# Kernel tuning notes

Hardware: AMD Instinct MI355X
Metric: run time of the kernel (lower is better)

## Reference

```python
import jax, jax.numpy as jnp
import numpy as np

N_NODES = 100000
BASE_DIM = 128
E1 = 500000
E2 = 250000
N_TYPES = 4


def setup_inputs() -> dict:
    key = jax.random.key(0)
    ks = jax.random.split(key, 9)
    x = jax.random.normal(ks[0], (N_NODES, BASE_DIM), dtype=jnp.float32)
    # per-edge-type dense transforms (shape-1: d->d, shape-2: 2d->d)
    W1 = jax.random.normal(ks[1], (N_TYPES, BASE_DIM, BASE_DIM), dtype=jnp.float32) * 0.05
    W2 = jax.random.normal(ks[2], (N_TYPES, 2 * BASE_DIM, BASE_DIM), dtype=jnp.float32) * 0.05
    src1 = jax.random.randint(ks[3], (E1,), 0, N_NODES, dtype=jnp.int32)
    tgt1 = jax.random.randint(ks[4], (E1,), 0, N_NODES, dtype=jnp.int32)
    type1 = jax.random.randint(ks[5], (E1,), 0, N_TYPES, dtype=jnp.int32)
    src2 = jax.random.randint(ks[6], (2 * E2,), 0, N_NODES, dtype=jnp.int32)
    tgt2 = jax.random.randint(ks[7], (E2,), 0, N_NODES, dtype=jnp.int32)
    type2 = jax.random.randint(ks[8], (E2,), 0, N_TYPES, dtype=jnp.int32)
    return {"x": x, "W1": W1, "W2": W2, "src1": src1, "tgt1": tgt1,
            "type1": type1, "src2": src2, "tgt2": tgt2, "type2": type2}


def _gather_transform_scatter(x, W, src, tgt, etype, arity, n_nodes):
    # gather `arity` source nodes per hyperedge and concat features: (E, arity*d)
    d = x.shape[1]
    concat = x[src].reshape(-1, arity * d)
    # per-edge-type dense transform; small loop over fixed #types, masked accumulate
    acc = jnp.zeros((concat.shape[0], d), dtype=x.dtype)
    for t in range(W.shape[0]):
        acc = acc + jnp.where((etype == t)[:, None], concat @ W[t], 0.0)
    # scatter-add messages to target nodes
    return jax.ops.segment_sum(acc, tgt, num_segments=n_nodes)


def reference(x, W1, W2, src1, tgt1, type1, src2, tgt2, type2):
    n = x.shape[0]
    out = x
    out = out + _gather_transform_scatter(x, W1, src1, tgt1, type1, 1, n)
    out = out + _gather_transform_scatter(x, W2, src2, tgt2, type2, 2, n)
    return out
```

## Files before the change

kernel.cpp:

```cpp
#include <hip/hip_runtime.h>
#include <hip/hip_bf16.h>

#define D 128
#define EPB 32
#define NB 256

typedef __attribute__((ext_vector_type(8))) short bf16x8;
typedef __attribute__((ext_vector_type(4))) float f32x4;

__device__ inline unsigned short f2bf(float f) {
    union { float f; unsigned int u; } v;
    v.f = f;
    unsigned int u = v.u;
    unsigned int r = u + 0x7fffu + ((u >> 16) & 1u);
    return (unsigned short)(r >> 16);
}
__device__ inline float bf2f(unsigned short b) {
    union { unsigned int u; float f; } v;
    v.u = ((unsigned int)b) << 16;
    return v.f;
}

__global__ __launch_bounds__(256) void copy_kernel(float* __restrict__ out,
                                                   const float* __restrict__ x,
                                                   int n_elems) {
    int n4 = n_elems >> 2;
    const float4* src = (const float4*)x;
    float4* dst = (float4*)out;
    for (int i = blockIdx.x * blockDim.x + threadIdx.x; i < n4;
         i += gridDim.x * blockDim.x)
        dst[i] = src[i];
}

__global__ __launch_bounds__(256) void conv_w(const float* __restrict__ W,
                                              unsigned short* __restrict__ Wt,
                                              int K) {
    __shared__ float tile[32][33];
    int k0 = blockIdx.x * 32, c0 = blockIdx.y * 32, t = blockIdx.z;
    int tr = threadIdx.x >> 5, tc = threadIdx.x & 31;
#pragma unroll
    for (int m = 0; m < 4; m++)
        tile[m * 8 + tr][tc] = W[((size_t)t * K + k0 + m * 8 + tr) * D + c0 + tc];
    __syncthreads();
#pragma unroll
    for (int m = 0; m < 4; m++)
        Wt[((size_t)t * D + c0 + m * 8 + tr) * K + k0 + tc] = f2bf(tile[tc][m * 8 + tr]);
}

__global__ __launch_bounds__(256) void hist_types(const int* __restrict__ type,
                                                  int n, int* __restrict__ hist) {
    __shared__ int h[4];
    if (threadIdx.x < 4) h[threadIdx.x] = 0;
    __syncthreads();
    for (int i = blockIdx.x * 256 + threadIdx.x; i < n; i += NB * 256)
        atomicAdd(&h[type[i]], 1);
    __syncthreads();
    if (threadIdx.x < 4) hist[blockIdx.x * 4 + threadIdx.x] = h[threadIdx.x];
}

__global__ void scan_offsets(int* __restrict__ meta,
                             const int* __restrict__ hist1, int* __restrict__ off1,
                             const int* __restrict__ hist2, int* __restrict__ off2) {
    int t = threadIdx.x;
    if (t < 4) {
        int s = 0;
        for (int b = 0; b < NB; b++) s += hist1[b * 4 + t];
        meta[t] = s;
    } else if (t < 8) {
        int tt = t - 4, s = 0;
        for (int b = 0; b < NB; b++) s += hist2[b * 4 + tt];
        meta[4 + tt] = s;
    }
    __syncthreads();
    if (t == 0) {
        int p = 0;
        for (int k = 0; k < 4; k++) {
            meta[8 + k] = p;
            p += ((meta[k] + EPB - 1) / EPB) * EPB;
        }
        meta[12] = p;
        p = 0;
        for (int k = 0; k < 4; k++) {
            meta[13 + k] = p;
            p += ((meta[4 + k] + EPB - 1) / EPB) * EPB;
        }
        meta[17] = p;
    }
    __syncthreads();
    if (t < 4) {
        int p = meta[8 + t];
        for (int b = 0; b < NB; b++) { off1[b * 4 + t] = p; p += hist1[b * 4 + t]; }
    } else if (t < 8) {
        int tt = t - 4;
        int p = meta[13 + tt];
        for (int b = 0; b < NB; b++) { off2[b * 4 + tt] = p; p += hist2[b * 4 + tt]; }
    }
}

__global__ __launch_bounds__(256) void write_sorted(const int* __restrict__ type,
                                                    int n,
                                                    const int* __restrict__ off,
                                                    int* __restrict__ sorted) {
    __shared__ int loff[4];
    if (threadIdx.x < 4) loff[threadIdx.x] = off[blockIdx.x * 4 + threadIdx.x];
    __syncthreads();
    for (int i = blockIdx.x * 256 + threadIdx.x; i < n; i += NB * 256) {
        int t = type[i];
        int pos = atomicAdd(&loff[t], 1);
        sorted[pos] = i;
    }
}

__global__ __launch_bounds__(256) void assign_rel(const int* __restrict__ tgt, int n,
                                                  int* __restrict__ cnt,
                                                  int* __restrict__ pos) {
    for (int i = blockIdx.x * blockDim.x + threadIdx.x; i < n;
         i += gridDim.x * blockDim.x)
        pos[i] = atomicAdd(&cnt[tgt[i]], 1);
}

__global__ __launch_bounds__(256) void scan_pass1(const int* __restrict__ cnt, int n,
                                                  int* __restrict__ base,
                                                  int* __restrict__ bsum) {
    __shared__ int s[256];
    int b = blockIdx.x, t = threadIdx.x;
    int i0 = b * 512 + 2 * t;
    int v0 = (i0 < n) ? cnt[i0] : 0;
    int v1 = (i0 + 1 < n) ? cnt[i0 + 1] : 0;
    s[t] = v0 + v1;
    __syncthreads();
    for (int off = 1; off < 256; off <<= 1) {
        int v = s[t];
        int u = (t >= off) ? s[t - off] : 0;
        __syncthreads();
        s[t] = v + u;
        __syncthreads();
    }
    int excl = (t > 0) ? s[t - 1] : 0;
    if (i0 < n) base[i0] = excl;
    if (i0 + 1 < n) base[i0 + 1] = excl + v0;
    if (t == 255) bsum[b] = s[255];
}

__global__ __launch_bounds__(256) void scan_pass2(int* __restrict__ bsum, int nb) {
    __shared__ int s[256];
    int t = threadIdx.x;
    int run = 0;
    for (int b0 = 0; b0 < nb; b0 += 256) {
        int v = (b0 + t < nb) ? bsum[b0 + t] : 0;
        s[t] = v;
        __syncthreads();
        for (int off = 1; off < 256; off <<= 1) {
            int a = s[t];
            int u = (t >= off) ? s[t - off] : 0;
            __syncthreads();
            s[t] = a + u;
            __syncthreads();
        }
        if (b0 + t < nb) bsum[b0 + t] = run + ((t > 0) ? s[t - 1] : 0);
        int tot = s[255];
        __syncthreads();
        run += tot;
    }
    if (t == 0) bsum[nb] = run;
}

__global__ __launch_bounds__(256) void scan_pass3(int* __restrict__ base,
                                                  const int* __restrict__ bsum, int n) {
    int i = blockIdx.x * 256 + threadIdx.x;
    if (i < n) base[i] += bsum[i >> 9];
    else if (i == n) base[n] = bsum[(n + 511) >> 9];
}

__global__ __launch_bounds__(256) void edge1_msg(
    const float* __restrict__ x, const unsigned short* __restrict__ Wt1,
    const int* __restrict__ src, const int* __restrict__ tgt,
    const int* __restrict__ sorted, const int* __restrict__ meta,
    const int* __restrict__ basep, const int* __restrict__ pos,
    unsigned short* __restrict__ msg) {
    __shared__ uint4 As4[512];
    __shared__ int s_mrow[EPB];
    __shared__ int s_src[EPB];
    char* As = (char*)As4;

    int tid = threadIdx.x;
    int g0 = blockIdx.x * EPB;
    const int* pb = meta + 8;
    int t = 0;
#pragma unroll
    for (int k = 1; k < 4; k++)
        if (g0 >= pb[k]) t = k;
    const unsigned short* __restrict__ W = Wt1 + (size_t)t * D * D;

    if (tid < EPB) {
        int eid = sorted[g0 + tid];
        int sv = -1, mr = -1;
        if (eid >= 0) { sv = src[eid]; mr = basep[tgt[eid]] + pos[eid]; }
        s_src[tid] = sv;
        s_mrow[tid] = mr;
    }
    __syncthreads();

    {
        int r = tid >> 3, u0 = tid & 7;
        int sv = s_src[r];
        const float4* srow = (const float4*)(x + (size_t)sv * D);
#pragma unroll
        for (int q = 0; q < 4; q++) {
            int u = u0 + 8 * q;
            float4 v = make_float4(0.f, 0.f, 0.f, 0.f);
            if (sv >= 0) v = srow[u];
            uint2 p;
            p.x = (unsigned)f2bf(v.x) | ((unsigned)f2bf(v.y) << 16);
            p.y = (unsigned)f2bf(v.z) | ((unsigned)f2bf(v.w) << 16);
            int byte = ((((u >> 1) * 16) ^ ((r & 7) << 4)) + (u & 1) * 8);
            *(uint2*)(As + r * 256 + byte) = p;
        }
    }
    __syncthreads();

    int wave = tid >> 6, lane = tid & 63;
    int c0 = wave * 32;
    int lrow = lane & 15, lgrp = lane >> 4;

    bf16x8 b[2][4];
#pragma unroll
    for (int fc = 0; fc < 2; fc++)
#pragma unroll
        for (int kk = 0; kk < 4; kk++)
            b[fc][kk] = *(const bf16x8*)(W + (size_t)(c0 + fc * 16 + lrow) * D +
                                         kk * 32 + lgrp * 8);

    f32x4 acc[2][2];
#pragma unroll
    for (int i = 0; i < 2; i++)
#pragma unroll
        for (int j = 0; j < 2; j++) acc[i][j] = (f32x4){0.f, 0.f, 0.f, 0.f};

#pragma unroll
    for (int kk = 0; kk < 4; kk++) {
        bf16x8 a0, a1;
        {
            int r = lrow;
            a0 = *(const bf16x8*)(As + r * 256 +
                                  ((kk * 64 + lgrp * 16) ^ ((r & 7) << 4)));
        }
        {
            int r = 16 + lrow;
            a1 = *(const bf16x8*)(As + r * 256 +
                                  ((kk * 64 + lgrp * 16) ^ ((r & 7) << 4)));
        }
        acc[0][0] = __builtin_amdgcn_mfma_f32_16x16x32_bf16(a0, b[0][kk], acc[0][0], 0, 0, 0);
        acc[1][0] = __builtin_amdgcn_mfma_f32_16x16x32_bf16(a1, b[0][kk], acc[1][0], 0, 0, 0);
        acc[0][1] = __builtin_amdgcn_mfma_f32_16x16x32_bf16(a0, b[1][kk], acc[0][1], 0, 0, 0);
        acc[1][1] = __builtin_amdgcn_mfma_f32_16x16x32_bf16(a1, b[1][kk], acc[1][1], 0, 0, 0);
    }

#pragma unroll
    for (int fr = 0; fr < 2; fr++)
#pragma unroll
        for (int reg = 0; reg < 4; reg++) {
            int erow = fr * 16 + lgrp * 4 + reg;
            int mr = s_mrow[erow];
            if (mr >= 0) {
#pragma unroll
                for (int fc = 0; fc < 2; fc++)
                    msg[(size_t)mr * D + c0 + fc * 16 + lrow] =
                        f2bf(acc[fr][fc][reg]);
            }
        }
}

__global__ __launch_bounds__(256) void edge2_msg(
    const float* __restrict__ x, const unsigned short* __restrict__ Wt2,
    const int* __restrict__ src2, const int* __restrict__ tgt,
    const int* __restrict__ sorted, const int* __restrict__ meta,
    const int* __restrict__ basep, const int* __restrict__ pos,
    unsigned short* __restrict__ msg) {
    __shared__ uint4 As4[1024];
    __shared__ int s_mrow[EPB];
    __shared__ int s_srcA[EPB];
    __shared__ int s_srcB[EPB];
    char* As = (char*)As4;

    int tid = threadIdx.x;
    int g0 = blockIdx.x * EPB;
    const int* pb = meta + 13;
    int t = 0;
#pragma unroll
    for (int k = 1; k < 4; k++)
        if (g0 >= pb[k]) t = k;
    const unsigned short* __restrict__ W = Wt2 + (size_t)t * D * 2 * D;

    if (tid < EPB) {
        int eid = sorted[g0 + tid];
        int sa = -1, sb = -1, mr = -1;
        if (eid >= 0) {
            sa = src2[2 * eid];
            sb = src2[2 * eid + 1];
            mr = basep[tgt[eid]] + pos[eid];
        }
        s_srcA[tid] = sa;
        s_srcB[tid] = sb;
        s_mrow[tid] = mr;
    }
    __syncthreads();

    {
        int r = tid >> 3, u0 = tid & 7;
        int sa = s_srcA[r], sb = s_srcB[r];
        const float4* rowA = (const float4*)(x + (size_t)sa * D);
        const float4* rowB = (const float4*)(x + (size_t)sb * D);
#pragma unroll
        for (int q = 0; q < 8; q++) {
            int u = u0 + 8 * q;
            float4 v = make_float4(0.f, 0.f, 0.f, 0.f);
            if (sa >= 0) v = (u < 32) ? rowA[u] : rowB[u - 32];
            uint2 p;
            p.x = (unsigned)f2bf(v.x) | ((unsigned)f2bf(v.y) << 16);
            p.y = (unsigned)f2bf(v.z) | ((unsigned)f2bf(v.w) << 16);
            int byte = ((((u >> 1) * 16) ^ ((r & 7) << 4)) + (u & 1) * 8);
            *(uint2*)(As + r * 512 + byte) = p;
        }
    }
    __syncthreads();

    int wave = tid >> 6, lane = tid & 63;
    int c0 = wave * 32;
    int lrow = lane & 15, lgrp = lane >> 4;

    f32x4 acc[2][2];
#pragma unroll
    for (int i = 0; i < 2; i++)
#pragma unroll
        for (int j = 0; j < 2; j++) acc[i][j] = (f32x4){0.f, 0.f, 0.f, 0.f};

#pragma unroll
    for (int kk = 0; kk < 8; kk++) {
        bf16x8 b0 = *(const bf16x8*)(W + (size_t)(c0 + lrow) * 2 * D + kk * 32 + lgrp * 8);
        bf16x8 b1 = *(const bf16x8*)(W + (size_t)(c0 + 16 + lrow) * 2 * D + kk * 32 + lgrp * 8);
        bf16x8 a0, a1;
        {
            int r = lrow;
            a0 = *(const bf16x8*)(As + r * 512 +
                                  ((kk * 64 + lgrp * 16) ^ ((r & 7) << 4)));
        }
        {
            int r = 16 + lrow;
            a1 = *(const bf16x8*)(As + r * 512 +
                                  ((kk * 64 + lgrp * 16) ^ ((r & 7) << 4)));
        }
        acc[0][0] = __builtin_amdgcn_mfma_f32_16x16x32_bf16(a0, b0, acc[0][0], 0, 0, 0);
        acc[1][0] = __builtin_amdgcn_mfma_f32_16x16x32_bf16(a1, b0, acc[1][0], 0, 0, 0);
        acc[0][1] = __builtin_amdgcn_mfma_f32_16x16x32_bf16(a0, b1, acc[0][1], 0, 0, 0);
        acc[1][1] = __builtin_amdgcn_mfma_f32_16x16x32_bf16(a1, b1, acc[1][1], 0, 0, 0);
    }

#pragma unroll
    for (int fr = 0; fr < 2; fr++)
#pragma unroll
        for (int reg = 0; reg < 4; reg++) {
            int erow = fr * 16 + lgrp * 4 + reg;
            int mr = s_mrow[erow];
            if (mr >= 0) {
#pragma unroll
                for (int fc = 0; fc < 2; fc++)
                    msg[(size_t)mr * D + c0 + fc * 16 + lrow] =
                        f2bf(acc[fr][fc][reg]);
            }
        }
}

__global__ __launch_bounds__(256) void finalize(
    const float* __restrict__ x, const unsigned short* __restrict__ msg,
    const int* __restrict__ basep, float* __restrict__ out, int nn) {
    int wib = threadIdx.x >> 6, lane = threadIdx.x & 63;
    for (int v = blockIdx.x * 4 + wib; v < nn; v += gridDim.x * 4) {
        int b0 = basep[v], b1 = basep[v + 1];
        float2 xv = *(const float2*)(x + (size_t)v * D + lane * 2);
        float a0 = xv.x, a1 = xv.y;
        for (int i = b0; i < b1; i++) {
            unsigned u = *(const unsigned*)(msg + (size_t)i * D + lane * 2);
            a0 += bf2f((unsigned short)(u & 0xffff));
            a1 += bf2f((unsigned short)(u >> 16));
        }
        *(float2*)(out + (size_t)v * D + lane * 2) = make_float2(a0, a1);
    }
}

__global__ __launch_bounds__(256) void edge1_mfma(
    const float* __restrict__ x, const unsigned short* __restrict__ Wt1,
    const int* __restrict__ src, const int* __restrict__ tgt,
    const int* __restrict__ sorted, const int* __restrict__ meta,
    float* __restrict__ out) {
    __shared__ uint4 As4[512];
    __shared__ int s_tgt[EPB];
    __shared__ int s_src[EPB];
    char* As = (char*)As4;

    int tid = threadIdx.x;
    int g0 = blockIdx.x * EPB;
    const int* pb = meta + 8;
    int t = 0;
#pragma unroll
    for (int k = 1; k < 4; k++)
        if (g0 >= pb[k]) t = k;
    const unsigned short* __restrict__ W = Wt1 + (size_t)t * D * D;

    if (tid < EPB) {
        int eid = sorted[g0 + tid];
        int sv = -1, tv = -1;
        if (eid >= 0) { sv = src[eid]; tv = tgt[eid]; }
        s_src[tid] = sv;
        s_tgt[tid] = tv;
    }
    __syncthreads();
    {
        int r = tid >> 3, u0 = tid & 7;
        int sv = s_src[r];
        const float4* srow = (const float4*)(x + (size_t)sv * D);
#pragma unroll
        for (int q = 0; q < 4; q++) {
            int u = u0 + 8 * q;
            float4 v = make_float4(0.f, 0.f, 0.f, 0.f);
            if (sv >= 0) v = srow[u];
            uint2 p;
            p.x = (unsigned)f2bf(v.x) | ((unsigned)f2bf(v.y) << 16);
            p.y = (unsigned)f2bf(v.z) | ((unsigned)f2bf(v.w) << 16);
            int byte = ((((u >> 1) * 16) ^ ((r & 7) << 4)) + (u & 1) * 8);
            *(uint2*)(As + r * 256 + byte) = p;
        }
    }
    __syncthreads();

    int wave = tid >> 6, lane = tid & 63;
    int c0 = wave * 32;
    int lrow = lane & 15, lgrp = lane >> 4;

    bf16x8 b[2][4];
#pragma unroll
    for (int fc = 0; fc < 2; fc++)
#pragma unroll
        for (int kk = 0; kk < 4; kk++)
            b[fc][kk] = *(const bf16x8*)(W + (size_t)(c0 + fc * 16 + lrow) * D +
                                         kk * 32 + lgrp * 8);

    f32x4 acc[2][2];
#pragma unroll
    for (int i = 0; i < 2; i++)
#pragma unroll
        for (int j = 0; j < 2; j++) acc[i][j] = (f32x4){0.f, 0.f, 0.f, 0.f};

#pragma unroll
    for (int kk = 0; kk < 4; kk++) {
        bf16x8 a0, a1;
        {
            int r = lrow;
            a0 = *(const bf16x8*)(As + r * 256 + ((kk * 64 + lgrp * 16) ^ ((r & 7) << 4)));
        }
        {
            int r = 16 + lrow;
            a1 = *(const bf16x8*)(As + r * 256 + ((kk * 64 + lgrp * 16) ^ ((r & 7) << 4)));
        }
        acc[0][0] = __builtin_amdgcn_mfma_f32_16x16x32_bf16(a0, b[0][kk], acc[0][0], 0, 0, 0);
        acc[1][0] = __builtin_amdgcn_mfma_f32_16x16x32_bf16(a1, b[0][kk], acc[1][0], 0, 0, 0);
        acc[0][1] = __builtin_amdgcn_mfma_f32_16x16x32_bf16(a0, b[1][kk], acc[0][1], 0, 0, 0);
        acc[1][1] = __builtin_amdgcn_mfma_f32_16x16x32_bf16(a1, b[1][kk], acc[1][1], 0, 0, 0);
    }

#pragma unroll
    for (int fr = 0; fr < 2; fr++)
#pragma unroll
        for (int reg = 0; reg < 4; reg++) {
            int erow = fr * 16 + lgrp * 4 + reg;
            int tv = s_tgt[erow];
            if (tv >= 0) {
#pragma unroll
                for (int fc = 0; fc < 2; fc++)
                    atomicAdd(&out[(size_t)tv * D + c0 + fc * 16 + lrow],
                              acc[fr][fc][reg]);
            }
        }
}

__global__ __launch_bounds__(256) void edge2_mfma(
    const float* __restrict__ x, const unsigned short* __restrict__ Wt2,
    const int* __restrict__ src2, const int* __restrict__ tgt,
    const int* __restrict__ sorted, const int* __restrict__ meta,
    float* __restrict__ out) {
    __shared__ uint4 As4[1024];
    __shared__ int s_tgt[EPB];
    __shared__ int s_srcA[EPB];
    __shared__ int s_srcB[EPB];
    char* As = (char*)As4;

    int tid = threadIdx.x;
    int g0 = blockIdx.x * EPB;
    const int* pb = meta + 13;
    int t = 0;
#pragma unroll
    for (int k = 1; k < 4; k++)
        if (g0 >= pb[k]) t = k;
    const unsigned short* __restrict__ W = Wt2 + (size_t)t * D * 2 * D;

    if (tid < EPB) {
        int eid = sorted[g0 + tid];
        int sa = -1, sb = -1, tv = -1;
        if (eid >= 0) { sa = src2[2 * eid]; sb = src2[2 * eid + 1]; tv = tgt[eid]; }
        s_srcA[tid] = sa;
        s_srcB[tid] = sb;
        s_tgt[tid] = tv;
    }
    __syncthreads();
    {
        int r = tid >> 3, u0 = tid & 7;
        int sa = s_srcA[r], sb = s_srcB[r];
        const float4* rowA = (const float4*)(x + (size_t)sa * D);
        const float4* rowB = (const float4*)(x + (size_t)sb * D);
#pragma unroll
        for (int q = 0; q < 8; q++) {
            int u = u0 + 8 * q;
            float4 v = make_float4(0.f, 0.f, 0.f, 0.f);
            if (sa >= 0) v = (u < 32) ? rowA[u] : rowB[u - 32];
            uint2 p;
            p.x = (unsigned)f2bf(v.x) | ((unsigned)f2bf(v.y) << 16);
            p.y = (unsigned)f2bf(v.z) | ((unsigned)f2bf(v.w) << 16);
            int byte = ((((u >> 1) * 16) ^ ((r & 7) << 4)) + (u & 1) * 8);
            *(uint2*)(As + r * 512 + byte) = p;
        }
    }
    __syncthreads();

    int wave = tid >> 6, lane = tid & 63;
    int c0 = wave * 32;
    int lrow = lane & 15, lgrp = lane >> 4;

    f32x4 acc[2][2];
#pragma unroll
    for (int i = 0; i < 2; i++)
#pragma unroll
        for (int j = 0; j < 2; j++) acc[i][j] = (f32x4){0.f, 0.f, 0.f, 0.f};

#pragma unroll
    for (int kk = 0; kk < 8; kk++) {
        bf16x8 b0 = *(const bf16x8*)(W + (size_t)(c0 + lrow) * 2 * D + kk * 32 + lgrp * 8);
        bf16x8 b1 = *(const bf16x8*)(W + (size_t)(c0 + 16 + lrow) * 2 * D + kk * 32 + lgrp * 8);
        bf16x8 a0, a1;
        {
            int r = lrow;
            a0 = *(const bf16x8*)(As + r * 512 + ((kk * 64 + lgrp * 16) ^ ((r & 7) << 4)));
        }
        {
            int r = 16 + lrow;
            a1 = *(const bf16x8*)(As + r * 512 + ((kk * 64 + lgrp * 16) ^ ((r & 7) << 4)));
        }
        acc[0][0] = __builtin_amdgcn_mfma_f32_16x16x32_bf16(a0, b0, acc[0][0], 0, 0, 0);
        acc[1][0] = __builtin_amdgcn_mfma_f32_16x16x32_bf16(a1, b0, acc[1][0], 0, 0, 0);
        acc[0][1] = __builtin_amdgcn_mfma_f32_16x16x32_bf16(a0, b1, acc[0][1], 0, 0, 0);
        acc[1][1] = __builtin_amdgcn_mfma_f32_16x16x32_bf16(a1, b1, acc[1][1], 0, 0, 0);
    }

#pragma unroll
    for (int fr = 0; fr < 2; fr++)
#pragma unroll
        for (int reg = 0; reg < 4; reg++) {
            int erow = fr * 16 + lgrp * 4 + reg;
            int tv = s_tgt[erow];
            if (tv >= 0) {
#pragma unroll
                for (int fc = 0; fc < 2; fc++)
                    atomicAdd(&out[(size_t)tv * D + c0 + fc * 16 + lrow],
                              acc[fr][fc][reg]);
            }
        }
}

__global__ __launch_bounds__(256) void e1_simple(
    const float* __restrict__ x, const float* __restrict__ W1,
    const int* __restrict__ src, const int* __restrict__ tgt,
    const int* __restrict__ type, float* __restrict__ out, int n) {
    int lane = threadIdx.x & 63;
    int wid = (blockIdx.x * blockDim.x + threadIdx.x) >> 6;
    int nw = (gridDim.x * blockDim.x) >> 6;
    for (int e = wid; e < n; e += nw) {
        const float* W = W1 + (size_t)type[e] * D * D;
        const float* xr = x + (size_t)src[e] * D;
        float a0 = 0.f, a1 = 0.f;
        for (int i = 0; i < D; i++) {
            float xv = xr[i];
            a0 = fmaf(xv, W[i * D + lane], a0);
            a1 = fmaf(xv, W[i * D + 64 + lane], a1);
        }
        atomicAdd(&out[(size_t)tgt[e] * D + lane], a0);
        atomicAdd(&out[(size_t)tgt[e] * D + 64 + lane], a1);
    }
}

__global__ __launch_bounds__(256) void e2_simple(
    const float* __restrict__ x, const float* __restrict__ W2,
    const int* __restrict__ src2, const int* __restrict__ tgt,
    const int* __restrict__ type, float* __restrict__ out, int n) {
    int lane = threadIdx.x & 63;
    int wid = (blockIdx.x * blockDim.x + threadIdx.x) >> 6;
    int nw = (gridDim.x * blockDim.x) >> 6;
    for (int e = wid; e < n; e += nw) {
        const float* W = W2 + (size_t)type[e] * 2 * D * D;
        const float* xrA = x + (size_t)src2[2 * e] * D;
        const float* xrB = x + (size_t)src2[2 * e + 1] * D;
        float a0 = 0.f, a1 = 0.f;
        for (int i = 0; i < 2 * D; i++) {
            float xv = (i < D) ? xrA[i] : xrB[i - D];
            a0 = fmaf(xv, W[i * D + lane], a0);
            a1 = fmaf(xv, W[i * D + 64 + lane], a1);
        }
        atomicAdd(&out[(size_t)tgt[e] * D + lane], a0);
        atomicAdd(&out[(size_t)tgt[e] * D + 64 + lane], a1);
    }
}

extern "C" void kernel_launch(void* const* d_in, const int* in_sizes, int n_in,
                              void* d_out, int out_size, void* d_ws, size_t ws_size,
                              hipStream_t stream) {
    const float* x = (const float*)d_in[0];
    const float* W1 = (const float*)d_in[1];
    const float* W2 = (const float*)d_in[2];
    const int* src1 = (const int*)d_in[3];
    const int* tgt1 = (const int*)d_in[4];
    const int* type1 = (const int*)d_in[5];
    const int* src2 = (const int*)d_in[6];
    const int* tgt2 = (const int*)d_in[7];
    const int* type2 = (const int*)d_in[8];
    float* out = (float*)d_out;

    int nn = in_sizes[0] / D;
    int E1c = in_sizes[3];
    int E2c = in_sizes[7];

    int grid1 = (E1c + 4 * (EPB - 1) + EPB - 1) / EPB;
    int grid2 = (E2c + 4 * (EPB - 1) + EPB - 1) / EPB;
    int cap1 = grid1 * EPB;
    int cap2 = grid2 * EPB;
    int nb_scan = (nn + 511) / 512;

    size_t o_meta = 0;
    size_t o_hist1 = o_meta + 32;
    size_t o_off1 = o_hist1 + (size_t)NB * 4;
    size_t o_hist2 = o_off1 + (size_t)NB * 4;
    size_t o_off2 = o_hist2 + (size_t)NB * 4;
    size_t o_sorted1 = o_off2 + (size_t)NB * 4;
    size_t o_sorted2 = o_sorted1 + cap1;
    size_t o_pos1 = o_sorted2 + cap2;
    size_t o_pos2 = o_pos1 + E1c;
    size_t o_cnt = o_pos2 + E2c;
    size_t o_base = o_cnt + nn;
    size_t o_bsum = o_base + nn + 1;
    size_t ints_full = o_bsum + nb_scan + 1;
    size_t ints_r3 = o_pos1;

    size_t w1_elems = (size_t)4 * D * D;
    size_t w2_elems = (size_t)4 * D * 2 * D;

    size_t wb_full = (ints_full * 4 + 255) & ~(size_t)255;
    size_t wb_r3 = (ints_r3 * 4 + 255) & ~(size_t)255;
    size_t wt_bytes = (w1_elems + w2_elems) * 2;

    size_t msg_off = (wb_full + wt_bytes + 255) & ~(size_t)255;
    size_t msg_bytes = (size_t)(E1c + E2c) * D * 2;
    size_t need_full = msg_off + msg_bytes;
    size_t need_r3 = wb_r3 + wt_bytes;

    if (ws_size >= need_full) {
        int* wsI = (int*)d_ws;
        int* meta = wsI + o_meta;
        int* hist1 = wsI + o_hist1;
        int* off1 = wsI + o_off1;
        int* hist2 = wsI + o_hist2;
        int* off2 = wsI + o_off2;
        int* sorted1 = wsI + o_sorted1;
        int* sorted2 = wsI + o_sorted2;
        int* pos1 = wsI + o_pos1;
        int* pos2 = wsI + o_pos2;
        int* cnt = wsI + o_cnt;
        int* basep = wsI + o_base;
        int* bsum = wsI + o_bsum;
        unsigned short* wt1 = (unsigned short*)((char*)d_ws + wb_full);
        unsigned short* wt2 = wt1 + w1_elems;
        unsigned short* msg = (unsigned short*)((char*)d_ws + msg_off);

        hipMemsetAsync(sorted1, 0xFF, (size_t)4 * (cap1 + cap2), stream);
        hipMemsetAsync(cnt, 0, (size_t)4 * nn, stream);

        conv_w<<<dim3(4, 4, 4), 256, 0, stream>>>(W1, wt1, D);
        conv_w<<<dim3(8, 4, 4), 256, 0, stream>>>(W2, wt2, 2 * D);

        hist_types<<<NB, 256, 0, stream>>>(type1, E1c, hist1);
        hist_types<<<NB, 256, 0, stream>>>(type2, E2c, hist2);
        scan_offsets<<<1, 64, 0, stream>>>(meta, hist1, off1, hist2, off2);
        write_sorted<<<NB, 256, 0, stream>>>(type1, E1c, off1, sorted1);
        write_sorted<<<NB, 256, 0, stream>>>(type2, E2c, off2, sorted2);

        assign_rel<<<2048, 256, 0, stream>>>(tgt1, E1c, cnt, pos1);
        assign_rel<<<2048, 256, 0, stream>>>(tgt2, E2c, cnt, pos2);
        scan_pass1<<<nb_scan, 256, 0, stream>>>(cnt, nn, basep, bsum);
        scan_pass2<<<1, 256, 0, stream>>>(bsum, nb_scan);
        scan_pass3<<<(nn + 1 + 255) / 256, 256, 0, stream>>>(basep, bsum, nn);

        edge1_msg<<<grid1, 256, 0, stream>>>(x, wt1, src1, tgt1, sorted1, meta,
                                             basep, pos1, msg);
        edge2_msg<<<grid2, 256, 0, stream>>>(x, wt2, src2, tgt2, sorted2, meta,
                                             basep, pos2, msg);

        finalize<<<(nn + 3) / 4, 256, 0, stream>>>(x, msg, basep, out, nn);
    } else if (ws_size >= need_r3) {
        int* wsI = (int*)d_ws;
        int* meta = wsI + o_meta;
        int* hist1 = wsI + o_hist1;
        int* off1 = wsI + o_off1;
        int* hist2 = wsI + o_hist2;
        int* off2 = wsI + o_off2;
        int* sorted1 = wsI + o_sorted1;
        int* sorted2 = wsI + o_sorted2;
        unsigned short* wt1 = (unsigned short*)((char*)d_ws + wb_r3);
        unsigned short* wt2 = wt1 + w1_elems;

        copy_kernel<<<2048, 256, 0, stream>>>(out, x, nn * D);
        hipMemsetAsync(sorted1, 0xFF, (size_t)4 * (cap1 + cap2), stream);

        conv_w<<<dim3(4, 4, 4), 256, 0, stream>>>(W1, wt1, D);
        conv_w<<<dim3(8, 4, 4), 256, 0, stream>>>(W2, wt2, 2 * D);

        hist_types<<<NB, 256, 0, stream>>>(type1, E1c, hist1);
        hist_types<<<NB, 256, 0, stream>>>(type2, E2c, hist2);
        scan_offsets<<<1, 64, 0, stream>>>(meta, hist1, off1, hist2, off2);
        write_sorted<<<NB, 256, 0, stream>>>(type1, E1c, off1, sorted1);
        write_sorted<<<NB, 256, 0, stream>>>(type2, E2c, off2, sorted2);

        edge1_mfma<<<grid1, 256, 0, stream>>>(x, wt1, src1, tgt1, sorted1, meta, out);
        edge2_mfma<<<grid2, 256, 0, stream>>>(x, wt2, src2, tgt2, sorted2, meta, out);
    } else {
        copy_kernel<<<2048, 256, 0, stream>>>(out, x, nn * D);
        e1_simple<<<2048, 256, 0, stream>>>(x, W1, src1, tgt1, type1, out, E1c);
        e2_simple<<<2048, 256, 0, stream>>>(x, W2, src2, tgt2, type2, out, E2c);
    }
}
```

Measured before the change: 344.0 us.

## Precompute per-node transformed tables for all types, then gather per target

Result: no change. 345.2 us (+0.3%).

```diff
diff --git a/kernel.cpp b/kernel.cpp
--- a/kernel.cpp
+++ b/kernel.cpp
@@ -20,6 +20,8 @@
     v.u = ((unsigned int)b) << 16;
     return v.f;
 }
+__device__ inline float bflo(unsigned u) { return bf2f((unsigned short)(u & 0xffff)); }
+__device__ inline float bfhi(unsigned u) { return bf2f((unsigned short)(u >> 16)); }
 
 __global__ __launch_bounds__(256) void copy_kernel(float* __restrict__ out,
                                                    const float* __restrict__ x,
@@ -172,6 +174,164 @@
     else if (i == n) base[n] = bsum[(n + 511) >> 9];
 }
 
+#define RMASK ((1 << 27) - 1)
+__global__ __launch_bounds__(256) void write_rec1(
+    const int* __restrict__ src, const int* __restrict__ tgt,
+    const int* __restrict__ type, int n, const int* __restrict__ base,
+    const int* __restrict__ pos, int* __restrict__ rec) {
+    for (int i = blockIdx.x * blockDim.x + threadIdx.x; i < n;
+         i += gridDim.x * blockDim.x)
+        rec[base[tgt[i]] + pos[i]] = src[i] | (type[i] << 27);
+}
+
+__global__ __launch_bounds__(256) void write_rec2(
+    const int* __restrict__ src2, const int* __restrict__ tgt,
+    const int* __restrict__ type, int n, const int* __restrict__ base,
+    const int* __restrict__ pos, int* __restrict__ reca, int* __restrict__ recb) {
+    for (int i = blockIdx.x * blockDim.x + threadIdx.x; i < n;
+         i += gridDim.x * blockDim.x) {
+        int s = base[tgt[i]] + pos[i];
+        reca[s] = src2[2 * i] | (type[i] << 27);
+        recb[s] = src2[2 * i + 1];
+    }
+}
+
+__global__ __launch_bounds__(256) void dense12(
+    const float* __restrict__ x, const unsigned short* __restrict__ wt1,
+    const unsigned short* __restrict__ wt2, unsigned short* __restrict__ tabs,
+    int nn) {
+    __shared__ uint4 As4[2048];
+    char* As = (char*)As4;
+    int tid = threadIdx.x;
+    int m0 = blockIdx.x * 128;
+
+    {
+        int r = tid >> 1;
+        int u0 = tid & 1;
+        int node = m0 + r;
+        bool ok = node < nn;
+        const float4* srow = (const float4*)(x + (size_t)node * D);
+#pragma unroll
+        for (int q = 0; q < 16; q++) {
+            int u = u0 + 2 * q;
+            float4 v = make_float4(0.f, 0.f, 0.f, 0.f);
+            if (ok) v = srow[u];
+            uint2 p;
+            p.x = (unsigned)f2bf(v.x) | ((unsigned)f2bf(v.y) << 16);
+            p.y = (unsigned)f2bf(v.z) | ((unsigned)f2bf(v.w) << 16);
+            int byte = ((((u >> 1) * 16) ^ ((r & 7) << 4)) + (u & 1) * 8);
+            *(uint2*)(As + r * 256 + byte) = p;
+        }
+    }
+    __syncthreads();
+
+    int wave = tid >> 6, lane = tid & 63;
+    int lrow = lane & 15, lgrp = lane >> 4;
+    int r0 = wave * 32;
+
+    bf16x8 a[2][4];
+#pragma unroll
+    for (int fr = 0; fr < 2; fr++)
+#pragma unroll
+        for (int kk = 0; kk < 4; kk++) {
+            int rr = r0 + fr * 16 + lrow;
+            a[fr][kk] = *(const bf16x8*)(As + rr * 256 +
+                                         ((kk * 64 + lgrp * 16) ^ ((rr & 7) << 4)));
+        }
+
+    for (int g = 0; g < 12; g++) {
+        int t = g & 3;
+        const unsigned short* W;
+        int K, koff;
+        if (g < 4) { W = wt1 + (size_t)t * D * D; K = D; koff = 0; }
+        else if (g < 8) { W = wt2 + (size_t)t * D * 2 * D; K = 2 * D; koff = 0; }
+        else { W = wt2 + (size_t)t * D * 2 * D; K = 2 * D; koff = D; }
+        unsigned short* tab = tabs + (size_t)g * nn * D;
+
+        for (int cf = 0; cf < 4; cf++) {
+            int c0 = cf * 32;
+            bf16x8 b[2][4];
+#pragma unroll
+            for (int fc = 0; fc < 2; fc++)
+#pragma unroll
+                for (int kk = 0; kk < 4; kk++)
+                    b[fc][kk] = *(const bf16x8*)(W + (size_t)(c0 + fc * 16 + lrow) * K +
+                                                 koff + kk * 32 + lgrp * 8);
+            f32x4 acc[2][2];
+#pragma unroll
+            for (int i = 0; i < 2; i++)
+#pragma unroll
+                for (int j = 0; j < 2; j++) acc[i][j] = (f32x4){0.f, 0.f, 0.f, 0.f};
+#pragma unroll
+            for (int kk = 0; kk < 4; kk++) {
+                acc[0][0] = __builtin_amdgcn_mfma_f32_16x16x32_bf16(a[0][kk], b[0][kk], acc[0][0], 0, 0, 0);
+                acc[1][0] = __builtin_amdgcn_mfma_f32_16x16x32_bf16(a[1][kk], b[0][kk], acc[1][0], 0, 0, 0);
+                acc[0][1] = __builtin_amdgcn_mfma_f32_16x16x32_bf16(a[0][kk], b[1][kk], acc[0][1], 0, 0, 0);
+                acc[1][1] = __builtin_amdgcn_mfma_f32_16x16x32_bf16(a[1][kk], b[1][kk], acc[1][1], 0, 0, 0);
+            }
+#pragma unroll
+            for (int fr = 0; fr < 2; fr++)
+#pragma unroll
+                for (int reg = 0; reg < 4; reg++) {
+                    int node = m0 + r0 + fr * 16 + lgrp * 4 + reg;
+                    if (node < nn) {
+#pragma unroll
+                        for (int fc = 0; fc < 2; fc++)
+                            tab[(size_t)node * D + c0 + fc * 16 + lrow] =
+                                f2bf(acc[fr][fc][reg]);
+                    }
+                }
+        }
+    }
+}
+
+__global__ __launch_bounds__(256) void gather_fin(
+    const float* __restrict__ x, const unsigned short* __restrict__ tabs,
+    const int* __restrict__ base1, const int* __restrict__ rec1,
+    const int* __restrict__ base2, const int* __restrict__ rec2a,
+    const int* __restrict__ rec2b, float* __restrict__ out, int nn) {
+    int wib = threadIdx.x >> 6, lane = threadIdx.x & 63;
+    for (int v = blockIdx.x * 4 + wib; v < nn; v += gridDim.x * 4) {
+        float2 xv = *(const float2*)(x + (size_t)v * D + lane * 2);
+        float a0 = xv.x, a1 = xv.y;
+
+        int b0 = base1[v], b1 = base1[v + 1];
+        int i = b0;
+        for (; i + 1 < b1; i += 2) {
+            int r0 = rec1[i], r1 = rec1[i + 1];
+            const unsigned short* p0 =
+                tabs + ((size_t)(unsigned)(r0 >> 27) * nn + (r0 & RMASK)) * D;
+            const unsigned short* p1 =
+                tabs + ((size_t)(unsigned)(r1 >> 27) * nn + (r1 & RMASK)) * D;
+            unsigned u0 = *(const unsigned*)(p0 + lane * 2);
+            unsigned u1 = *(const unsigned*)(p1 + lane * 2);
+            a0 += bflo(u0) + bflo(u1);
+            a1 += bfhi(u0) + bfhi(u1);
+        }
+        if (i < b1) {
+            int r0 = rec1[i];
+            const unsigned short* p0 =
+                tabs + ((size_t)(unsigned)(r0 >> 27) * nn + (r0 & RMASK)) * D;
+            unsigned u0 = *(const unsigned*)(p0 + lane * 2);
+            a0 += bflo(u0);
+            a1 += bfhi(u0);
+        }
+
+        int c0 = base2[v], c1 = base2[v + 1];
+        for (int j = c0; j < c1; j++) {
+            int ra = rec2a[j], sb = rec2b[j];
+            int t = (int)((unsigned)ra >> 27), sa = ra & RMASK;
+            const unsigned short* pu = tabs + ((size_t)(4 + t) * nn + sa) * D;
+            const unsigned short* pl = tabs + ((size_t)(8 + t) * nn + sb) * D;
+            unsigned uu = *(const unsigned*)(pu + lane * 2);
+            unsigned ul = *(const unsigned*)(pl + lane * 2);
+            a0 += bflo(uu) + bflo(ul);
+            a1 += bfhi(uu) + bfhi(ul);
+        }
+        *(float2*)(out + (size_t)v * D + lane * 2) = make_float2(a0, a1);
+    }
+}
+
 __global__ __launch_bounds__(256) void edge1_msg(
     const float* __restrict__ x, const unsigned short* __restrict__ Wt1,
     const int* __restrict__ src, const int* __restrict__ tgt,
@@ -200,7 +360,6 @@
         s_mrow[tid] = mr;
     }
     __syncthreads();
-
     {
         int r = tid >> 3, u0 = tid & 7;
         int sv = s_src[r];
@@ -242,13 +401,11 @@
         bf16x8 a0, a1;
         {
             int r = lrow;
-            a0 = *(const bf16x8*)(As + r * 256 +
-                                  ((kk * 64 + lgrp * 16) ^ ((r & 7) << 4)));
+            a0 = *(const bf16x8*)(As + r * 256 + ((kk * 64 + lgrp * 16) ^ ((r & 7) << 4)));
         }
         {
             int r = 16 + lrow;
-            a1 = *(const bf16x8*)(As + r * 256 +
-                                  ((kk * 64 + lgrp * 16) ^ ((r & 7) << 4)));
+            a1 = *(const bf16x8*)(As + r * 256 + ((kk * 64 + lgrp * 16) ^ ((r & 7) << 4)));
         }
         acc[0][0] = __builtin_amdgcn_mfma_f32_16x16x32_bf16(a0, b[0][kk], acc[0][0], 0, 0, 0);
         acc[1][0] = __builtin_amdgcn_mfma_f32_16x16x32_bf16(a1, b[0][kk], acc[1][0], 0, 0, 0);
@@ -265,8 +422,7 @@
             if (mr >= 0) {
 #pragma unroll
                 for (int fc = 0; fc < 2; fc++)
-                    msg[(size_t)mr * D + c0 + fc * 16 + lrow] =
-                        f2bf(acc[fr][fc][reg]);
+                    msg[(size_t)mr * D + c0 + fc * 16 + lrow] = f2bf(acc[fr][fc][reg]);
             }
         }
 }
@@ -305,7 +461,6 @@
         s_mrow[tid] = mr;
     }
     __syncthreads();
-
     {
         int r = tid >> 3, u0 = tid & 7;
         int sa = s_srcA[r], sb = s_srcB[r];
@@ -342,13 +497,11 @@
         bf16x8 a0, a1;
         {
             int r = lrow;
-            a0 = *(const bf16x8*)(As + r * 512 +
-                                  ((kk * 64 + lgrp * 16) ^ ((r & 7) << 4)));
+            a0 = *(const bf16x8*)(As + r * 512 + ((kk * 64 + lgrp * 16) ^ ((r & 7) << 4)));
         }
         {
             int r = 16 + lrow;
-            a1 = *(const bf16x8*)(As + r * 512 +
-                                  ((kk * 64 + lgrp * 16) ^ ((r & 7) << 4)));
+            a1 = *(const bf16x8*)(As + r * 512 + ((kk * 64 + lgrp * 16) ^ ((r & 7) << 4)));
         }
         acc[0][0] = __builtin_amdgcn_mfma_f32_16x16x32_bf16(a0, b0, acc[0][0], 0, 0, 0);
         acc[1][0] = __builtin_amdgcn_mfma_f32_16x16x32_bf16(a1, b0, acc[1][0], 0, 0, 0);
@@ -365,8 +518,7 @@
             if (mr >= 0) {
 #pragma unroll
                 for (int fc = 0; fc < 2; fc++)
-                    msg[(size_t)mr * D + c0 + fc * 16 + lrow] =
-                        f2bf(acc[fr][fc][reg]);
+                    msg[(size_t)mr * D + c0 + fc * 16 + lrow] = f2bf(acc[fr][fc][reg]);
             }
         }
 }
@@ -381,198 +533,11 @@
         float a0 = xv.x, a1 = xv.y;
         for (int i = b0; i < b1; i++) {
             unsigned u = *(const unsigned*)(msg + (size_t)i * D + lane * 2);
-            a0 += bf2f((unsigned short)(u & 0xffff));
-            a1 += bf2f((unsigned short)(u >> 16));
+            a0 += bflo(u);
+            a1 += bfhi(u);
         }
         *(float2*)(out + (size_t)v * D + lane * 2) = make_float2(a0, a1);
     }
-}
-
-__global__ __launch_bounds__(256) void edge1_mfma(
-    const float* __restrict__ x, const unsigned short* __restrict__ Wt1,
-    const int* __restrict__ src, const int* __restrict__ tgt,
-    const int* __restrict__ sorted, const int* __restrict__ meta,
-    float* __restrict__ out) {
-    __shared__ uint4 As4[512];
-    __shared__ int s_tgt[EPB];
-    __shared__ int s_src[EPB];
-    char* As = (char*)As4;
-
-    int tid = threadIdx.x;
-    int g0 = blockIdx.x * EPB;
-    const int* pb = meta + 8;
-    int t = 0;
-#pragma unroll
-    for (int k = 1; k < 4; k++)
-        if (g0 >= pb[k]) t = k;
-    const unsigned short* __restrict__ W = Wt1 + (size_t)t * D * D;
-
-    if (tid < EPB) {
-        int eid = sorted[g0 + tid];
-        int sv = -1, tv = -1;
-        if (eid >= 0) { sv = src[eid]; tv = tgt[eid]; }
-        s_src[tid] = sv;
-        s_tgt[tid] = tv;
-    }
-    __syncthreads();
-    {
-        int r = tid >> 3, u0 = tid & 7;
-        int sv = s_src[r];
-        const float4* srow = (const float4*)(x + (size_t)sv * D);
-#pragma unroll
-        for (int q = 0; q < 4; q++) {
-            int u = u0 + 8 * q;
-            float4 v = make_float4(0.f, 0.f, 0.f, 0.f);
-            if (sv >= 0) v = srow[u];
-            uint2 p;
-            p.x = (unsigned)f2bf(v.x) | ((unsigned)f2bf(v.y) << 16);
-            p.y = (unsigned)f2bf(v.z) | ((unsigned)f2bf(v.w) << 16);
-            int byte = ((((u >> 1) * 16) ^ ((r & 7) << 4)) + (u & 1) * 8);
-            *(uint2*)(As + r * 256 + byte) = p;
-        }
-    }
-    __syncthreads();
-
-    int wave = tid >> 6, lane = tid & 63;
-    int c0 = wave * 32;
-    int lrow = lane & 15, lgrp = lane >> 4;
-
-    bf16x8 b[2][4];
-#pragma unroll
-    for (int fc = 0; fc < 2; fc++)
-#pragma unroll
-        for (int kk = 0; kk < 4; kk++)
-            b[fc][kk] = *(const bf16x8*)(W + (size_t)(c0 + fc * 16 + lrow) * D +
-                                         kk * 32 + lgrp * 8);
-
-    f32x4 acc[2][2];
-#pragma unroll
-    for (int i = 0; i < 2; i++)
-#pragma unroll
-        for (int j = 0; j < 2; j++) acc[i][j] = (f32x4){0.f, 0.f, 0.f, 0.f};
-
-#pragma unroll
-    for (int kk = 0; kk < 4; kk++) {
-        bf16x8 a0, a1;
-        {
-            int r = lrow;
-            a0 = *(const bf16x8*)(As + r * 256 + ((kk * 64 + lgrp * 16) ^ ((r & 7) << 4)));
-        }
-        {
-            int r = 16 + lrow;
-            a1 = *(const bf16x8*)(As + r * 256 + ((kk * 64 + lgrp * 16) ^ ((r & 7) << 4)));
-        }
-        acc[0][0] = __builtin_amdgcn_mfma_f32_16x16x32_bf16(a0, b[0][kk], acc[0][0], 0, 0, 0);
-        acc[1][0] = __builtin_amdgcn_mfma_f32_16x16x32_bf16(a1, b[0][kk], acc[1][0], 0, 0, 0);
-        acc[0][1] = __builtin_amdgcn_mfma_f32_16x16x32_bf16(a0, b[1][kk], acc[0][1], 0, 0, 0);
-        acc[1][1] = __builtin_amdgcn_mfma_f32_16x16x32_bf16(a1, b[1][kk], acc[1][1], 0, 0, 0);
-    }
-
-#pragma unroll
-    for (int fr = 0; fr < 2; fr++)
-#pragma unroll
-        for (int reg = 0; reg < 4; reg++) {
-            int erow = fr * 16 + lgrp * 4 + reg;
-            int tv = s_tgt[erow];
-            if (tv >= 0) {
-#pragma unroll
-                for (int fc = 0; fc < 2; fc++)
-                    atomicAdd(&out[(size_t)tv * D + c0 + fc * 16 + lrow],
-                              acc[fr][fc][reg]);
-            }
-        }
-}
-
-__global__ __launch_bounds__(256) void edge2_mfma(
-    const float* __restrict__ x, const unsigned short* __restrict__ Wt2,
-    const int* __restrict__ src2, const int* __restrict__ tgt,
-    const int* __restrict__ sorted, const int* __restrict__ meta,
-    float* __restrict__ out) {
-    __shared__ uint4 As4[1024];
-    __shared__ int s_tgt[EPB];
-    __shared__ int s_srcA[EPB];
-    __shared__ int s_srcB[EPB];
-    char* As = (char*)As4;
-
-    int tid = threadIdx.x;
-    int g0 = blockIdx.x * EPB;
-    const int* pb = meta + 13;
-    int t = 0;
-#pragma unroll
-    for (int k = 1; k < 4; k++)
-        if (g0 >= pb[k]) t = k;
-    const unsigned short* __restrict__ W = Wt2 + (size_t)t * D * 2 * D;
-
-    if (tid < EPB) {
-        int eid = sorted[g0 + tid];
-        int sa = -1, sb = -1, tv = -1;
-        if (eid >= 0) { sa = src2[2 * eid]; sb = src2[2 * eid + 1]; tv = tgt[eid]; }
-        s_srcA[tid] = sa;
-        s_srcB[tid] = sb;
-        s_tgt[tid] = tv;
-    }
-    __syncthreads();
-    {
-        int r = tid >> 3, u0 = tid & 7;
-        int sa = s_srcA[r], sb = s_srcB[r];
-        const float4* rowA = (const float4*)(x + (size_t)sa * D);
-        const float4* rowB = (const float4*)(x + (size_t)sb * D);
-#pragma unroll
-        for (int q = 0; q < 8; q++) {
-            int u = u0 + 8 * q;
-            float4 v = make_float4(0.f, 0.f, 0.f, 0.f);
-            if (sa >= 0) v = (u < 32) ? rowA[u] : rowB[u - 32];
-            uint2 p;
-            p.x = (unsigned)f2bf(v.x) | ((unsigned)f2bf(v.y) << 16);
-            p.y = (unsigned)f2bf(v.z) | ((unsigned)f2bf(v.w) << 16);
-            int byte = ((((u >> 1) * 16) ^ ((r & 7) << 4)) + (u & 1) * 8);
-            *(uint2*)(As + r * 512 + byte) = p;
-        }
-    }
-    __syncthreads();
-
-    int wave = tid >> 6, lane = tid & 63;
-    int c0 = wave * 32;
-    int lrow = lane & 15, lgrp = lane >> 4;
-
-    f32x4 acc[2][2];
-#pragma unroll
-    for (int i = 0; i < 2; i++)
-#pragma unroll
-        for (int j = 0; j < 2; j++) acc[i][j] = (f32x4){0.f, 0.f, 0.f, 0.f};
-
-#pragma unroll
-    for (int kk = 0; kk < 8; kk++) {
-        bf16x8 b0 = *(const bf16x8*)(W + (size_t)(c0 + lrow) * 2 * D + kk * 32 + lgrp * 8);
-        bf16x8 b1 = *(const bf16x8*)(W + (size_t)(c0 + 16 + lrow) * 2 * D + kk * 32 + lgrp * 8);
-        bf16x8 a0, a1;
-        {
-            int r = lrow;
-            a0 = *(const bf16x8*)(As + r * 512 + ((kk * 64 + lgrp * 16) ^ ((r & 7) << 4)));
-        }
-        {
-            int r = 16 + lrow;
-            a1 = *(const bf16x8*)(As + r * 512 + ((kk * 64 + lgrp * 16) ^ ((r & 7) << 4)));
-        }
-        acc[0][0] = __builtin_amdgcn_mfma_f32_16x16x32_bf16(a0, b0, acc[0][0], 0, 0, 0);
-        acc[1][0] = __builtin_amdgcn_mfma_f32_16x16x32_bf16(a1, b0, acc[1][0], 0, 0, 0);
-        acc[0][1] = __builtin_amdgcn_mfma_f32_16x16x32_bf16(a0, b1, acc[0][1], 0, 0, 0);
-        acc[1][1] = __builtin_amdgcn_mfma_f32_16x16x32_bf16(a1, b1, acc[1][1], 0, 0, 0);
-    }
-
-#pragma unroll
-    for (int fr = 0; fr < 2; fr++)
-#pragma unroll
-        for (int reg = 0; reg < 4; reg++) {
-            int erow = fr * 16 + lgrp * 4 + reg;
-            int tv = s_tgt[erow];
-            if (tv >= 0) {
-#pragma unroll
-                for (int fc = 0; fc < 2; fc++)
-                    atomicAdd(&out[(size_t)tv * D + c0 + fc * 16 + lrow],
-                              acc[fr][fc][reg]);
-            }
-        }
 }
 
 __global__ __launch_bounds__(256) void e1_simple(
@@ -636,12 +601,32 @@
     int E1c = in_sizes[3];
     int E2c = in_sizes[7];
 
+    int nb_scan = (nn + 511) / 512;
+    size_t w1_elems = (size_t)4 * D * D;
+    size_t w2_elems = (size_t)4 * D * 2 * D;
+    size_t wt_bytes = (w1_elems + w2_elems) * 2;
+
+    size_t o_cnt1 = 0;
+    size_t o_cnt2 = o_cnt1 + nn;
+    size_t o_base1 = o_cnt2 + nn;
+    size_t o_base2 = o_base1 + nn + 1;
+    size_t o_bsum1 = o_base2 + nn + 1;
+    size_t o_bsum2 = o_bsum1 + nb_scan + 1;
+    size_t o_pos1d = o_bsum2 + nb_scan + 1;
+    size_t o_pos2d = o_pos1d + E1c;
+    size_t o_rec1 = o_pos2d + E2c;
+    size_t o_rec2a = o_rec1 + E1c;
+    size_t o_rec2b = o_rec2a + E2c;
+    size_t ints_dense = o_rec2b + E2c;
+    size_t wtd_off = (ints_dense * 4 + 255) & ~(size_t)255;
+    size_t tab_off = (wtd_off + wt_bytes + 255) & ~(size_t)255;
+    size_t tab_bytes = (size_t)12 * nn * D * 2;
+    size_t need_dense = tab_off + tab_bytes;
+
     int grid1 = (E1c + 4 * (EPB - 1) + EPB - 1) / EPB;
     int grid2 = (E2c + 4 * (EPB - 1) + EPB - 1) / EPB;
     int cap1 = grid1 * EPB;
     int cap2 = grid2 * EPB;
-    int nb_scan = (nn + 511) / 512;
-
     size_t o_meta = 0;
     size_t o_hist1 = o_meta + 32;
     size_t o_off1 = o_hist1 + (size_t)NB * 4;
@@ -656,20 +641,54 @@
     size_t o_bsum = o_base + nn + 1;
     size_t ints_full = o_bsum + nb_scan + 1;
     size_t ints_r3 = o_pos1;
-
-    size_t w1_elems = (size_t)4 * D * D;
-    size_t w2_elems = (size_t)4 * D * 2 * D;
-
     size_t wb_full = (ints_full * 4 + 255) & ~(size_t)255;
     size_t wb_r3 = (ints_r3 * 4 + 255) & ~(size_t)255;
-    size_t wt_bytes = (w1_elems + w2_elems) * 2;
-
     size_t msg_off = (wb_full + wt_bytes + 255) & ~(size_t)255;
     size_t msg_bytes = (size_t)(E1c + E2c) * D * 2;
     size_t need_full = msg_off + msg_bytes;
     size_t need_r3 = wb_r3 + wt_bytes;
 
-    if (ws_size >= need_full) {
+    if (ws_size >= need_dense && nn < (1 << 27)) {
+        int* wsI = (int*)d_ws;
+        int* cnt1 = wsI + o_cnt1;
+        int* cnt2 = wsI + o_cnt2;
+        int* base1 = wsI + o_base1;
+        int* base2 = wsI + o_base2;
+        int* bsum1 = wsI + o_bsum1;
+        int* bsum2 = wsI + o_bsum2;
+        int* pos1 = wsI + o_pos1d;
+        int* pos2 = wsI + o_pos2d;
+        int* rec1 = wsI + o_rec1;
+        int* rec2a = wsI + o_rec2a;
+        int* rec2b = wsI + o_rec2b;
+        unsigned short* wt1 = (unsigned short*)((char*)d_ws + wtd_off);
+        unsigned short* wt2 = wt1 + w1_elems;
+        unsigned short* tabs = (unsigned short*)((char*)d_ws + tab_off);
+
+        hipMemsetAsync(cnt1, 0, (size_t)8 * nn, stream);
+
+        conv_w<<<dim3(4, 4, 4), 256, 0, stream>>>(W1, wt1, D);
+        conv_w<<<dim3(8, 4, 4), 256, 0, stream>>>(W2, wt2, 2 * D);
+
+        assign_rel<<<2048, 256, 0, stream>>>(tgt1, E1c, cnt1, pos1);
+        assign_rel<<<2048, 256, 0, stream>>>(tgt2, E2c, cnt2, pos2);
+
+        scan_pass1<<<nb_scan, 256, 0, stream>>>(cnt1, nn, base1, bsum1);
+        scan_pass2<<<1, 256, 0, stream>>>(bsum1, nb_scan);
+        scan_pass3<<<(nn + 1 + 255) / 256, 256, 0, stream>>>(base1, bsum1, nn);
+        scan_pass1<<<nb_scan, 256, 0, stream>>>(cnt2, nn, base2, bsum2);
+        scan_pass2<<<1, 256, 0, stream>>>(bsum2, nb_scan);
+        scan_pass3<<<(nn + 1 + 255) / 256, 256, 0, stream>>>(base2, bsum2, nn);
+
+        write_rec1<<<2048, 256, 0, stream>>>(src1, tgt1, type1, E1c, base1, pos1, rec1);
+        write_rec2<<<2048, 256, 0, stream>>>(src2, tgt2, type2, E2c, base2, pos2,
+                                             rec2a, rec2b);
+
+        dense12<<<(nn + 127) / 128, 256, 0, stream>>>(x, wt1, wt2, tabs, nn);
+
+        gather_fin<<<(nn + 3) / 4, 256, 0, stream>>>(x, tabs, base1, rec1, base2,
+                                                     rec2a, rec2b, out, nn);
+    } else if (ws_size >= need_full) {
         int* wsI = (int*)d_ws;
         int* meta = wsI + o_meta;
         int* hist1 = wsI + o_hist1;
@@ -709,34 +728,7 @@
                                              basep, pos1, msg);
         edge2_msg<<<grid2, 256, 0, stream>>>(x, wt2, src2, tgt2, sorted2, meta,
                                              basep, pos2, msg);
-
         finalize<<<(nn + 3) / 4, 256, 0, stream>>>(x, msg, basep, out, nn);
-    } else if (ws_size >= need_r3) {
-        int* wsI = (int*)d_ws;
-        int* meta = wsI + o_meta;
-        int* hist1 = wsI + o_hist1;
-        int* off1 = wsI + o_off1;
-        int* hist2 = wsI + o_hist2;
-        int* off2 = wsI + o_off2;
-        int* sorted1 = wsI + o_sorted1;
-        int* sorted2 = wsI + o_sorted2;
-        unsigned short* wt1 = (unsigned short*)((char*)d_ws + wb_r3);
-        unsigned short* wt2 = wt1 + w1_elems;
-
-        copy_kernel<<<2048, 256, 0, stream>>>(out, x, nn * D);
-        hipMemsetAsync(sorted1, 0xFF, (size_t)4 * (cap1 + cap2), stream);
-
-        conv_w<<<dim3(4, 4, 4), 256, 0, stream>>>(W1, wt1, D);
-        conv_w<<<dim3(8, 4, 4), 256, 0, stream>>>(W2, wt2, 2 * D);
-
-        hist_types<<<NB, 256, 0, stream>>>(type1, E1c, hist1);
-        hist_types<<<NB, 256, 0, stream>>>(type2, E2c, hist2);
-        scan_offsets<<<1, 64, 0, stream>>>(meta, hist1, off1, hist2, off2);
-        write_sorted<<<NB, 256, 0, stream>>>(type1, E1c, off1, sorted1);
-        write_sorted<<<NB, 256, 0, stream>>>(type2, E2c, off2, sorted2);
-
-        edge1_mfma<<<grid1, 256, 0, stream>>>(x, wt1, src1, tgt1, sorted1, meta, out);
-        edge2_mfma<<<grid2, 256, 0, stream>>>(x, wt2, src2, tgt2, sorted2, meta, out);
     } else {
         copy_kernel<<<2048, 256, 0, stream>>>(out, x, nn * D);
         e1_simple<<<2048, 256, 0, stream>>>(x, W1, src1, tgt1, type1, out, E1c);
```
